# Kernel tuning notes

Measured on AMD Instinct MI355X. Metric: run time of the kernel, lower is better.

The kernel has to match this reference:

```python
import jax, jax.numpy as jnp
import numpy as np

N_NODES = 50000
N_EDGES = 800000
N_GRAPHS = 64
IN_CH = 128
HID = 128
PROC_X = 128
Q_DIM = 768
PROC_Q = 128
OUT_CH = 32


def setup_inputs() -> dict:
    key = jax.random.key(0)
    ks = jax.random.split(key, 16)
    inp = {
        "x": jax.random.normal(ks[0], (N_NODES, IN_CH), dtype=jnp.float32),
        "edge_index": jax.random.randint(ks[1], (2, N_EDGES), 0, N_NODES, dtype=jnp.int64),
        "batch": jnp.sort(jax.random.randint(ks[2], (N_NODES,), 0, N_GRAPHS, dtype=jnp.int64)),
        "question_embedding": jax.random.normal(ks[3], (N_GRAPHS, Q_DIM), dtype=jnp.float32),
    }
    s = 1.0 / np.sqrt(HID)
    inp["W0"] = jax.random.uniform(ks[4], (IN_CH, HID), minval=-s, maxval=s)
    inp["b0"] = jnp.zeros((HID,), jnp.float32)
    inp["W1"] = jax.random.uniform(ks[5], (HID, HID), minval=-s, maxval=s)
    inp["b1"] = jnp.zeros((HID,), jnp.float32)
    inp["W2"] = jax.random.uniform(ks[6], (HID, PROC_X), minval=-s, maxval=s)
    inp["b2"] = jnp.zeros((PROC_X,), jnp.float32)
    inp["fc0_w"] = jax.random.uniform(ks[7], (Q_DIM, PROC_Q), minval=-s, maxval=s)
    inp["fc0_b"] = jnp.zeros((PROC_Q,), jnp.float32)
    inp["fc1_w"] = jax.random.uniform(ks[8], (PROC_X + PROC_Q, HID), minval=-s, maxval=s)
    inp["fc1_b"] = jnp.zeros((HID,), jnp.float32)
    inp["fc2_w"] = jax.random.uniform(ks[9], (HID, OUT_CH), minval=-s, maxval=s)
    inp["fc2_b"] = jnp.zeros((OUT_CH,), jnp.float32)
    return inp


def _gcn_norm(edge_index, n_nodes):
    """Add self-loops and compute symmetric GCN normalization per edge."""
    loop = jnp.arange(n_nodes, dtype=edge_index.dtype)
    src = jnp.concatenate([edge_index[0], loop])
    dst = jnp.concatenate([edge_index[1], loop])
    ones = jnp.ones_like(dst, dtype=jnp.float32)
    deg = jax.ops.segment_sum(ones, dst, num_segments=n_nodes)
    dinv = jnp.where(deg > 0, jax.lax.rsqrt(deg), 0.0)
    norm = dinv[src] * dinv[dst]  # [E+N]
    return src, dst, norm


def _gcn_conv(x, src, dst, norm, W, b):
    h = x @ W                                # [N, F_out]
    msg = h[src] * norm[:, None]             # gather + scale  [E+N, F_out]
    agg = jax.ops.segment_sum(msg, dst, num_segments=x.shape[0])
    return agg + b


def reference(x, edge_index, batch, question_embedding,
              W0, b0, W1, b1, W2, b2,
              fc0_w, fc0_b, fc1_w, fc1_b, fc2_w, fc2_b):
    n = x.shape[0]
    src, dst, norm = _gcn_norm(edge_index, n)
    h = jax.nn.relu(_gcn_conv(x, src, dst, norm, W0, b0))
    h = jax.nn.relu(_gcn_conv(h, src, dst, norm, W1, b1))
    h = jax.nn.relu(_gcn_conv(h, src, dst, norm, W2, b2))
    q = jax.nn.relu(question_embedding @ fc0_w + fc0_b)  # [G, PROC_Q]
    q_exp = q[batch]                                      # [N, PROC_Q]
    combined = jnp.concatenate([h, q_exp], axis=1)
    out = jax.nn.relu(combined @ fc1_w + fc1_b)
    out = out @ fc2_w + fc2_b
    return out
```

## Files before the change

kernel.cpp:

```cpp
#include <hip/hip_runtime.h>
#include <hip/hip_bf16.h>

#define N_NODES 50000
#define N_EDGES 800000
#define N_GRAPHS 64
#define LSTR 136

typedef __attribute__((ext_vector_type(4))) short s4v;
typedef __attribute__((ext_vector_type(8))) short s8v;
typedef __attribute__((ext_vector_type(16))) float f16v;

struct HL { short hi, lo; };

__device__ inline HL bsplit(float f) {
    HL r;
    unsigned u = __float_as_uint(f);
    unsigned rh = (u + 0x7FFFu + ((u >> 16) & 1u)) >> 16;
    r.hi = (short)rh;
    float fh = __uint_as_float(rh << 16);
    float fl = f - fh;
    unsigned u2 = __float_as_uint(fl);
    unsigned rl = (u2 + 0x7FFFu + ((u2 >> 16) & 1u)) >> 16;
    r.lo = (short)rl;
    return r;
}

__device__ inline unsigned short f2bf(float f) {
    unsigned u = __float_as_uint(f);
    return (unsigned short)((u + 0x7FFFu + ((u >> 16) & 1u)) >> 16);
}

__device__ inline float bflo(unsigned u) { return __uint_as_float(u << 16); }
__device__ inline float bfhi(unsigned u) { return __uint_as_float(u & 0xFFFF0000u); }

__device__ inline void gat8(const unsigned* __restrict__ Hs,
                            const unsigned short* __restrict__ colA,
                            int e, int l, float& a0, float& a1) {
    uint4 cw = *(const uint4*)(colA + e);
    unsigned u0 = Hs[(cw.x & 0xFFFFu) * 64u + l];
    unsigned u1 = Hs[(cw.x >> 16) * 64u + l];
    unsigned u2 = Hs[(cw.y & 0xFFFFu) * 64u + l];
    unsigned u3 = Hs[(cw.y >> 16) * 64u + l];
    unsigned u4 = Hs[(cw.z & 0xFFFFu) * 64u + l];
    unsigned u5 = Hs[(cw.z >> 16) * 64u + l];
    unsigned u6 = Hs[(cw.w & 0xFFFFu) * 64u + l];
    unsigned u7 = Hs[(cw.w >> 16) * 64u + l];
    a0 += ((bflo(u0) + bflo(u1)) + (bflo(u2) + bflo(u3)))
        + ((bflo(u4) + bflo(u5)) + (bflo(u6) + bflo(u7)));
    a1 += ((bfhi(u0) + bfhi(u1)) + (bfhi(u2) + bfhi(u3)))
        + ((bfhi(u4) + bfhi(u5)) + (bfhi(u6) + bfhi(u7)));
}


__global__ void k_hist(const int* __restrict__ ei, int* __restrict__ cnt,
                       int* __restrict__ rank, int E) {
    int e = blockIdx.x * 256 + threadIdx.x;
    if (e < E) rank[e] = atomicAdd(&cnt[ei[E + e]], 1);
}

__global__ __launch_bounds__(512) void k_scan_a(const int* __restrict__ cnt,
                                                int* __restrict__ rowptr,
                                                int* __restrict__ bsum,
                                                float* __restrict__ dinv, int n) {
    __shared__ int s[512];
    int t = threadIdx.x;
    int i = blockIdx.x * 512 + t;
    int v = (i < n) ? cnt[i] : 0;
    if (i < n) dinv[i] = rsqrtf((float)(v + 1));
    int pv = (v + 7) & ~7;
    s[t] = pv;
    __syncthreads();
    for (int d = 1; d < 512; d <<= 1) {
        int x = (t >= d) ? s[t - d] : 0;
        __syncthreads();
        s[t] += x;
        __syncthreads();
    }
    if (i < n) rowptr[i] = s[t] - pv;
    if (t == 511) bsum[blockIdx.x] = s[511];
}

__global__ __launch_bounds__(512) void k_scan_c(int* __restrict__ rowptr,
                                                const int* __restrict__ bsum,
                                                int n, int nb) {
    __shared__ int sb[128];
    int t = threadIdx.x;
    if (t < 128) sb[t] = (t < nb) ? bsum[t] : 0;
    __syncthreads();
    for (int d = 1; d < 128; d <<= 1) {
        int x = 0;
        if (t < 128 && t >= d) x = sb[t - d];
        __syncthreads();
        if (t < 128) sb[t] += x;
        __syncthreads();
    }
    int add = (blockIdx.x > 0) ? sb[blockIdx.x - 1] : 0;
    int i = blockIdx.x * 512 + t;
    if (i < n) rowptr[i] += add;
    if (i == 0) rowptr[n] = sb[nb - 1];
}

__global__ void k_fill_csr(const int* __restrict__ ei, const int* __restrict__ rowptr,
                           const int* __restrict__ rank,
                           unsigned short* __restrict__ colA, int E) {
    int e = blockIdx.x * 256 + threadIdx.x;
    if (e >= E) return;
    colA[rowptr[ei[E + e]] + rank[e]] = (unsigned short)ei[e];
}

__global__ __launch_bounds__(512) void k_prep(const float* __restrict__ qe,
                                              const float* __restrict__ fc0w,
                                              const float* __restrict__ fc0b,
                                              const float* __restrict__ fc1w,
                                              const float* __restrict__ fc1b,
                                              const float* __restrict__ W0,
                                              const float* __restrict__ W1,
                                              const float* __restrict__ W2,
                                              const float* __restrict__ fc2w,
                                              short* __restrict__ WH,
                                              short* __restrict__ WL,
                                              int* __restrict__ cntz,
                                              unsigned* __restrict__ Hsd,
                                              unsigned* __restrict__ Hsd2,
                                              unsigned short* __restrict__ colA,
                                              float* __restrict__ qq) {
    int b = blockIdx.x, tid = threadIdx.x;
    if (b >= 225) {
        int idx = (b - 225) * 512 + tid;
        if (idx < 143752) {
            uint4 p;
            p.x = p.y = p.z = p.w = 0xC350C350u;
            ((uint4*)colA)[idx] = p;
        }
        return;
    }
    if (b >= 200) {
        int idx = (b - 200) * 512 + tid;
        if (idx < 12504) ((int4*)cntz)[idx] = make_int4(0, 0, 0, 0);
        if (b == 200 && tid < 64) {
            Hsd[(unsigned)N_NODES * 64u + tid] = 0u;
            Hsd2[(unsigned)N_NODES * 64u + tid] = 0u;
        }
        return;
    }
    if (b >= 64) {
        int i = (b - 64) * 512 + tid;
        float val;
        int dst;
        if (i < 65536) {
            int mat = i >> 14, off = i & 16383;
            int k = off >> 7, n = off & 127;
            const float* src = (mat == 0) ? W0 : (mat == 1) ? W1 : (mat == 2) ? W2 : fc1w;
            val = src[k * 128 + n];
            dst = mat * 16384 + n * 128 + k;
        } else {
            int off = i - 65536;
            int k = off >> 5, n = off & 31;
            val = fc2w[k * 32 + n];
            dst = 65536 + n * 128 + k;
        }
        HL r = bsplit(val);
        WH[dst] = r.hi;
        WL[dst] = r.lo;
        return;
    }
    __shared__ float qs[768];
    __shared__ float red[512];
    __shared__ float ql[128];
    const float* fc1bot = fc1w + 128 * 128;
    int g = b;
    for (int i = tid; i < 768; i += 512) qs[i] = qe[g * 768 + i];
    __syncthreads();
    int j = tid & 127, sl = tid >> 7;
    int kb = sl * 192;
    float a0 = 0, a1 = 0, a2 = 0, a3 = 0;
    for (int k = 0; k < 192; k += 4) {
        a0 += qs[kb + k + 0] * fc0w[(kb + k + 0) * 128 + j];
        a1 += qs[kb + k + 1] * fc0w[(kb + k + 1) * 128 + j];
        a2 += qs[kb + k + 2] * fc0w[(kb + k + 2) * 128 + j];
        a3 += qs[kb + k + 3] * fc0w[(kb + k + 3) * 128 + j];
    }
    red[tid] = (a0 + a1) + (a2 + a3);
    __syncthreads();
    if (tid < 128)
        ql[tid] = fmaxf(((red[tid] + red[tid + 128]) + (red[tid + 256] + red[tid + 384]))
                        + fc0b[tid], 0.f);
    __syncthreads();
    kb = sl * 32;
    float b0 = 0, b1 = 0;
    for (int k = 0; k < 32; k += 2) {
        b0 += ql[kb + k + 0] * fc1bot[(kb + k + 0) * 128 + j];
        b1 += ql[kb + k + 1] * fc1bot[(kb + k + 1) * 128 + j];
    }
    red[tid] = b0 + b1;
    __syncthreads();
    if (tid < 128)
        qq[g * 128 + tid] = ((red[tid] + red[tid + 128]) + (red[tid + 256] + red[tid + 384]))
                            + fc1b[tid];
}

__global__ __launch_bounds__(128) void gemm_mf(const float* __restrict__ A32,
                                               const short* __restrict__ WTh,
                                               const short* __restrict__ WTl,
                                               const float* __restrict__ dinv,
                                               unsigned short* __restrict__ oHs,
                                               int nrows) {
    __shared__ short Ah[32 * LSTR];
    const int tid = threadIdx.x;
    const int row0 = blockIdx.x * 32;

    #pragma unroll
    for (int i = 0; i < 8; ++i) {
        int u = i * 128 + tid;
        int r = u >> 5, c4 = u & 31;
        int gr = row0 + r;
        float4 v = make_float4(0.f, 0.f, 0.f, 0.f);
        if (gr < nrows) v = ((const float4*)A32)[(size_t)gr * 32 + c4];
        s4v h4 = {(short)f2bf(v.x), (short)f2bf(v.y), (short)f2bf(v.z), (short)f2bf(v.w)};
        *(s4v*)&Ah[r * LSTR + c4 * 4] = h4;
    }
    __syncthreads();

    const int wv = tid >> 6, lane = tid & 63;
    const int m = lane & 31, half = lane >> 5;
    const int c0 = wv * 64 + m;
    f16v acc0 = {0.f}, acc1 = {0.f};
    #pragma unroll
    for (int ks = 0; ks < 8; ++ks) {
        int ko = ks * 16 + half * 8;
        s8v ah  = *(const s8v*)&Ah[m * LSTR + ko];
        s8v bh0 = *(const s8v*)&WTh[(size_t)c0 * 128 + ko];
        s8v bl0 = *(const s8v*)&WTl[(size_t)c0 * 128 + ko];
        s8v bh1 = *(const s8v*)&WTh[(size_t)(c0 + 32) * 128 + ko];
        s8v bl1 = *(const s8v*)&WTl[(size_t)(c0 + 32) * 128 + ko];
        acc0 = __builtin_amdgcn_mfma_f32_32x32x16_bf16(ah, bh0, acc0, 0, 0, 0);
        acc0 = __builtin_amdgcn_mfma_f32_32x32x16_bf16(ah, bl0, acc0, 0, 0, 0);
        acc1 = __builtin_amdgcn_mfma_f32_32x32x16_bf16(ah, bh1, acc1, 0, 0, 0);
        acc1 = __builtin_amdgcn_mfma_f32_32x32x16_bf16(ah, bl1, acc1, 0, 0, 0);
    }

    #pragma unroll
    for (int reg = 0; reg < 16; ++reg) {
        int rl = (reg & 3) + 8 * (reg >> 2) + 4 * half;
        int gr = row0 + rl;
        if (gr >= nrows) continue;
        float sc = dinv[gr];
        oHs[(size_t)gr * 128 + c0]      = f2bf(acc0[reg] * sc);
        oHs[(size_t)gr * 128 + c0 + 32] = f2bf(acc1[reg] * sc);
    }
}

template <int FC>
__global__ __launch_bounds__(512) void k_gg(const unsigned* __restrict__ Hs,
                                            const int* __restrict__ rowptr,
                                            const unsigned short* __restrict__ colA,
                                            const float* __restrict__ dinv,
                                            const float* __restrict__ bias,
                                            const short* __restrict__ WTh,
                                            const short* __restrict__ WTl,
                                            const short* __restrict__ W2h,
                                            const short* __restrict__ W2l,
                                            const float* __restrict__ qq,
                                            const int* __restrict__ batch,
                                            const float* __restrict__ fc2b,
                                            unsigned short* __restrict__ oHs,
                                            float* __restrict__ out,
                                            int n) {
    __shared__ short Ah[32 * LSTR];
    __shared__ short Pl[FC ? 32 * LSTR : 1];
    __shared__ float red[FC ? 3 * 32 * 33 : 1];
    const int tid = threadIdx.x;
    const int row0 = blockIdx.x * 32;
    const int wv = tid >> 6, l = tid & 63;
    const int m = l & 31, half = l >> 5;

    const float2 bb = ((const float2*)bias)[l];
    for (int i = 0; i < 4; ++i) {
        int r = wv * 4 + i;
        int node = row0 + r;
        unsigned pack = 0;
        if (node < n) {
            int e0 = __builtin_amdgcn_readfirstlane(rowptr[node]);
            int e1 = __builtin_amdgcn_readfirstlane(rowptr[node + 1]);
            float a0 = 0.f, a1 = 0.f;
            for (int e = e0; e < e1; e += 8)
                gat8(Hs, colA, e, l, a0, a1);
            float di = dinv[node];
            unsigned uh = Hs[(unsigned)node * 64u + l];
            float o0 = fmaxf((a0 + bflo(uh)) * di + bb.x, 0.f);
            float o1 = fmaxf((a1 + bfhi(uh)) * di + bb.y, 0.f);
            pack = (unsigned)f2bf(o0) | ((unsigned)f2bf(o1) << 16);
        }
        ((unsigned*)Ah)[r * 68 + l] = pack;
    }
    __syncthreads();

    const int c0 = wv * 32 + m;
    f16v acc = {0.f};
    if (wv < 4) {
        #pragma unroll
        for (int ks = 0; ks < 8; ++ks) {
            int ko = ks * 16 + half * 8;
            s8v ah = *(const s8v*)&Ah[m * LSTR + ko];
            s8v bh = *(const s8v*)&WTh[(size_t)c0 * 128 + ko];
            s8v bl = *(const s8v*)&WTl[(size_t)c0 * 128 + ko];
            acc = __builtin_amdgcn_mfma_f32_32x32x16_bf16(ah, bh, acc, 0, 0, 0);
            acc = __builtin_amdgcn_mfma_f32_32x32x16_bf16(ah, bl, acc, 0, 0, 0);
        }
    }

    if (FC == 0) {
        if (wv < 4) {
            #pragma unroll
            for (int reg = 0; reg < 16; ++reg) {
                int rl = (reg & 3) + 8 * (reg >> 2) + 4 * half;
                int gr = row0 + rl;
                if (gr >= n) continue;
                oHs[(size_t)gr * 128 + c0] = f2bf(acc[reg] * dinv[gr]);
            }
        }
    } else {
        __syncthreads();
        if (wv < 4) {
            #pragma unroll
            for (int reg = 0; reg < 16; ++reg) {
                int rl = (reg & 3) + 8 * (reg >> 2) + 4 * half;
                int gr = row0 + rl;
                int g = (gr < n) ? batch[gr] : 0;
                float v = fmaxf(acc[reg] + qq[(size_t)g * 128 + c0], 0.f);
                HL p = bsplit(v);
                Ah[rl * LSTR + c0] = p.hi;
                Pl[rl * LSTR + c0] = p.lo;
            }
        }
        __syncthreads();
        f16v acc2 = {0.f};
        if (wv < 4) {
            #pragma unroll
            for (int ks = 0; ks < 2; ++ks) {
                int ko = wv * 32 + ks * 16 + half * 8;
                s8v ah = *(const s8v*)&Ah[m * LSTR + ko];
                s8v al = *(const s8v*)&Pl[m * LSTR + ko];
                s8v bh = *(const s8v*)&W2h[(size_t)m * 128 + ko];
                s8v bl = *(const s8v*)&W2l[(size_t)m * 128 + ko];
                acc2 = __builtin_amdgcn_mfma_f32_32x32x16_bf16(ah, bh, acc2, 0, 0, 0);
                acc2 = __builtin_amdgcn_mfma_f32_32x32x16_bf16(ah, bl, acc2, 0, 0, 0);
                acc2 = __builtin_amdgcn_mfma_f32_32x32x16_bf16(al, bh, acc2, 0, 0, 0);
            }
            if (wv > 0) {
                #pragma unroll
                for (int reg = 0; reg < 16; ++reg) {
                    int rl = (reg & 3) + 8 * (reg >> 2) + 4 * half;
                    red[(wv - 1) * 1056 + rl * 33 + m] = acc2[reg];
                }
            }
        }
        __syncthreads();
        if (wv == 0) {
            #pragma unroll
            for (int reg = 0; reg < 16; ++reg) {
                int rl = (reg & 3) + 8 * (reg >> 2) + 4 * half;
                int gr = row0 + rl;
                if (gr < n)
                    out[(size_t)gr * 32 + m] = acc2[reg]
                        + (red[rl * 33 + m] + red[1056 + rl * 33 + m])
                        + red[2112 + rl * 33 + m] + fc2b[m];
            }
        }
    }
}


extern "C" void kernel_launch(void* const* d_in, const int* in_sizes, int n_in,
                              void* d_out, int out_size, void* d_ws, size_t ws_size,
                              hipStream_t stream) {
    const float* x    = (const float*)d_in[0];
    const int*   ei   = (const int*)d_in[1];
    const int*   batch= (const int*)d_in[2];
    const float* qe   = (const float*)d_in[3];
    const float* W0   = (const float*)d_in[4];
    const float* b0   = (const float*)d_in[5];
    const float* W1   = (const float*)d_in[6];
    const float* b1   = (const float*)d_in[7];
    const float* W2   = (const float*)d_in[8];
    const float* b2   = (const float*)d_in[9];
    const float* fc0w = (const float*)d_in[10];
    const float* fc0b = (const float*)d_in[11];
    const float* fc1w = (const float*)d_in[12];
    const float* fc1b = (const float*)d_in[13];
    const float* fc2w = (const float*)d_in[14];
    const float* fc2b = (const float*)d_in[15];
    float* out = (float*)d_out;

    float* WS = (float*)d_ws;
    unsigned short* HS  = (unsigned short*)WS;
    unsigned short* HS2 = (unsigned short*)(WS + 3200064);
    float* DINV = WS + 6400128;
    float* QQ   = WS + 6450144;
    int*   CNT  = (int*)(WS + 6458336);
    int*   ROWPTR = (int*)(WS + 6508352);
    int*   RANK = (int*)(WS + 6558368);
    unsigned short* COL = (unsigned short*)(WS + 7358368);
    int*   BSUM = (int*)(WS + 7933376);
    short* WTH  = (short*)(WS + 7933504);
    short* WTL  = WTH + 69632;

    const int N = N_NODES, E = N_EDGES;
    const int eb = (E + 255) / 256;
    const int sb = (N + 511) / 512;
    const int gg = (N + 31) / 32;

    k_prep<<<506, 512, 0, stream>>>(qe, fc0w, fc0b, fc1w, fc1b, W0, W1, W2, fc2w,
                                    WTH, WTL, CNT, (unsigned*)HS, (unsigned*)HS2, COL, QQ);
    k_hist<<<eb, 256, 0, stream>>>(ei, CNT, RANK, E);
    k_scan_a<<<sb, 512, 0, stream>>>(CNT, ROWPTR, BSUM, DINV, N);
    k_scan_c<<<sb, 512, 0, stream>>>(ROWPTR, BSUM, N, sb);
    k_fill_csr<<<eb, 256, 0, stream>>>(ei, ROWPTR, RANK, COL, E);

    gemm_mf<<<gg, 128, 0, stream>>>(x, WTH, WTL, DINV, HS, N);
    k_gg<0><<<gg, 512, 0, stream>>>((const unsigned*)HS, ROWPTR, COL, DINV, b0,
                                    WTH + 16384, WTL + 16384, nullptr, nullptr,
                                    nullptr, nullptr, nullptr, HS2, nullptr, N);
    k_gg<0><<<gg, 512, 0, stream>>>((const unsigned*)HS2, ROWPTR, COL, DINV, b1,
                                    WTH + 32768, WTL + 32768, nullptr, nullptr,
                                    nullptr, nullptr, nullptr, HS, nullptr, N);
    k_gg<1><<<gg, 512, 0, stream>>>((const unsigned*)HS, ROWPTR, COL, DINV, b2,
                                    WTH + 49152, WTL + 49152, WTH + 65536, WTL + 65536,
                                    QQ, batch, fc2b, nullptr, out, N);
}
```

Measured before the change: 319.3 us.

## Merge histogram into prep kernel and CSR fill into first GEMM; split gather accumulators

The edge histogram becomes extra blocks of the prep kernel, with the count zeroing moved to a memset beforehand. The CSR column fill becomes extra blocks of the first GEMM kernel, which removes two launches and lets independent work overlap. The gather loop now processes 16 edges per iteration into two independent accumulator pairs to expose more memory-level parallelism. A risk is the race between hist blocks and colA padding fill inside the same prep launch, but they touch different buffers, so ordering is preserved. The HS2 sentinel zero is dropped, which relies on padding indices only reading HS.

```diff
diff --git a/kernel.cpp b/kernel.cpp
--- a/kernel.cpp
+++ b/kernel.cpp
@@ -52,12 +52,6 @@
 }
 
 
-__global__ void k_hist(const int* __restrict__ ei, int* __restrict__ cnt,
-                       int* __restrict__ rank, int E) {
-    int e = blockIdx.x * 256 + threadIdx.x;
-    if (e < E) rank[e] = atomicAdd(&cnt[ei[E + e]], 1);
-}
-
 __global__ __launch_bounds__(512) void k_scan_a(const int* __restrict__ cnt,
                                                 int* __restrict__ rowptr,
                                                 int* __restrict__ bsum,
@@ -100,14 +94,6 @@
     if (i == 0) rowptr[n] = sb[nb - 1];
 }
 
-__global__ void k_fill_csr(const int* __restrict__ ei, const int* __restrict__ rowptr,
-                           const int* __restrict__ rank,
-                           unsigned short* __restrict__ colA, int E) {
-    int e = blockIdx.x * 256 + threadIdx.x;
-    if (e >= E) return;
-    colA[rowptr[ei[E + e]] + rank[e]] = (unsigned short)ei[e];
-}
-
 __global__ __launch_bounds__(512) void k_prep(const float* __restrict__ qe,
                                               const float* __restrict__ fc0w,
                                               const float* __restrict__ fc0b,
@@ -117,29 +103,30 @@
                                               const float* __restrict__ W1,
                                               const float* __restrict__ W2,
                                               const float* __restrict__ fc2w,
+                                              const int* __restrict__ ei,
+                                              int* __restrict__ cnt,
+                                              int* __restrict__ rank,
                                               short* __restrict__ WH,
                                               short* __restrict__ WL,
-                                              int* __restrict__ cntz,
                                               unsigned* __restrict__ Hsd,
-                                              unsigned* __restrict__ Hsd2,
                                               unsigned short* __restrict__ colA,
-                                              float* __restrict__ qq) {
+                                              float* __restrict__ qq, int E) {
     int b = blockIdx.x, tid = threadIdx.x;
-    if (b >= 225) {
-        int idx = (b - 225) * 512 + tid;
+    if (b >= 482) {
+        int e = (b - 482) * 512 + tid;
+        if (e < E) rank[e] = atomicAdd(&cnt[ei[E + e]], 1);
+        return;
+    }
+    if (b == 481) {
+        if (tid < 64) Hsd[(unsigned)N_NODES * 64u + tid] = 0u;
+        return;
+    }
+    if (b >= 200) {
+        int idx = (b - 200) * 512 + tid;
         if (idx < 143752) {
             uint4 p;
             p.x = p.y = p.z = p.w = 0xC350C350u;
             ((uint4*)colA)[idx] = p;
-        }
-        return;
-    }
-    if (b >= 200) {
-        int idx = (b - 200) * 512 + tid;
-        if (idx < 12504) ((int4*)cntz)[idx] = make_int4(0, 0, 0, 0);
-        if (b == 200 && tid < 64) {
-            Hsd[(unsigned)N_NODES * 64u + tid] = 0u;
-            Hsd2[(unsigned)N_NODES * 64u + tid] = 0u;
         }
         return;
     }
@@ -199,14 +186,23 @@
                             + fc1b[tid];
 }
 
-__global__ __launch_bounds__(128) void gemm_mf(const float* __restrict__ A32,
-                                               const short* __restrict__ WTh,
-                                               const short* __restrict__ WTl,
-                                               const float* __restrict__ dinv,
-                                               unsigned short* __restrict__ oHs,
-                                               int nrows) {
+__global__ __launch_bounds__(128) void k_fg(const float* __restrict__ A32,
+                                            const short* __restrict__ WTh,
+                                            const short* __restrict__ WTl,
+                                            const float* __restrict__ dinv,
+                                            unsigned short* __restrict__ oHs,
+                                            const int* __restrict__ ei,
+                                            const int* __restrict__ rowptr,
+                                            const int* __restrict__ rank,
+                                            unsigned short* __restrict__ colA,
+                                            int nrows, int E, int GG) {
+    const int tid = threadIdx.x;
+    if (blockIdx.x >= GG) {
+        int e = (blockIdx.x - GG) * 128 + tid;
+        if (e < E) colA[rowptr[ei[E + e]] + rank[e]] = (unsigned short)ei[e];
+        return;
+    }
     __shared__ short Ah[32 * LSTR];
-    const int tid = threadIdx.x;
     const int row0 = blockIdx.x * 32;
 
     #pragma unroll
@@ -282,9 +278,16 @@
         if (node < n) {
             int e0 = __builtin_amdgcn_readfirstlane(rowptr[node]);
             int e1 = __builtin_amdgcn_readfirstlane(rowptr[node + 1]);
-            float a0 = 0.f, a1 = 0.f;
-            for (int e = e0; e < e1; e += 8)
+            float a0 = 0.f, a1 = 0.f, c0v = 0.f, c1v = 0.f;
+            int e = e0;
+            for (; e + 16 <= e1; e += 16) {
                 gat8(Hs, colA, e, l, a0, a1);
+                gat8(Hs, colA, e + 8, l, c0v, c1v);
+            }
+            for (; e < e1; e += 8)
+                gat8(Hs, colA, e, l, a0, a1);
+            a0 += c0v;
+            a1 += c1v;
             float di = dinv[node];
             unsigned uh = Hs[(unsigned)node * 64u + l];
             float o0 = fmaxf((a0 + bflo(uh)) * di + bb.x, 0.f);
@@ -406,18 +409,19 @@
     short* WTL  = WTH + 69632;
 
     const int N = N_NODES, E = N_EDGES;
-    const int eb = (E + 255) / 256;
     const int sb = (N + 511) / 512;
     const int gg = (N + 31) / 32;
-
-    k_prep<<<506, 512, 0, stream>>>(qe, fc0w, fc0b, fc1w, fc1b, W0, W1, W2, fc2w,
-                                    WTH, WTL, CNT, (unsigned*)HS, (unsigned*)HS2, COL, QQ);
-    k_hist<<<eb, 256, 0, stream>>>(ei, CNT, RANK, E);
+    const int histb = (E + 511) / 512;
+    const int fillb = (E + 127) / 128;
+
+    (void)hipMemsetAsync(CNT, 0, N * sizeof(int), stream);
+    k_prep<<<482 + histb, 512, 0, stream>>>(qe, fc0w, fc0b, fc1w, fc1b,
+                                            W0, W1, W2, fc2w, ei, CNT, RANK,
+                                            WTH, WTL, (unsigned*)HS, COL, QQ, E);
     k_scan_a<<<sb, 512, 0, stream>>>(CNT, ROWPTR, BSUM, DINV, N);
     k_scan_c<<<sb, 512, 0, stream>>>(ROWPTR, BSUM, N, sb);
-    k_fill_csr<<<eb, 256, 0, stream>>>(ei, ROWPTR, RANK, COL, E);
-
-    gemm_mf<<<gg, 128, 0, stream>>>(x, WTH, WTL, DINV, HS, N);
+    k_fg<<<gg + fillb, 128, 0, stream>>>(x, WTH, WTL, DINV, HS,
+                                         ei, ROWPTR, RANK, COL, N, E, gg);
     k_gg<0><<<gg, 512, 0, stream>>>((const unsigned*)HS, ROWPTR, COL, DINV, b0,
                                     WTH + 16384, WTL + 16384, nullptr, nullptr,
                                     nullptr, nullptr, nullptr, HS2, nullptr, N);
```

Result: faster. 312.3 us (-2.2%).
